# Kernel tuning notes

Hardware: AMD Instinct MI355X
Metric: run time of the kernel (lower is better)

Reference implementation:

```python
import jax, jax.numpy as jnp
import numpy as np
import math

HIDDEN = 1024
HEADS = 16
HEAD_DIM = HIDDEN // HEADS


def setup_inputs() -> dict:
    key = jax.random.key(0)
    ks = jax.random.split(key, 9)
    B, T, C = 4, 2048, HIDDEN
    s = 0.02
    x = jax.random.normal(ks[0], (B, T, C), dtype=jnp.float32)
    # torch nn.Linear weights are [out_features, in_features]
    Wq = jax.random.normal(ks[1], (C, C), dtype=jnp.float32) * s
    Wk = jax.random.normal(ks[2], (C, C), dtype=jnp.float32) * s
    Wv = jax.random.normal(ks[3], (C, C), dtype=jnp.float32) * s
    Wo = jax.random.normal(ks[4], (C, C), dtype=jnp.float32) * s
    bq = jax.random.normal(ks[5], (C,), dtype=jnp.float32) * s
    bk = jax.random.normal(ks[6], (C,), dtype=jnp.float32) * s
    bv = jax.random.normal(ks[7], (C,), dtype=jnp.float32) * s
    bo = jax.random.normal(ks[8], (C,), dtype=jnp.float32) * s
    return {"x": x, "Wq": Wq, "bq": bq, "Wk": Wk, "bk": bk,
            "Wv": Wv, "bv": bv, "Wo": Wo, "bo": bo}


def reference(x, Wq, bq, Wk, bk, Wv, bv, Wo, bo):
    B, T, C = x.shape
    H, D = HEADS, HEAD_DIM
    # projections: torch Linear => x @ W.T + b
    q = (x @ Wq.T + bq).reshape(B, T, H, D).transpose(0, 2, 1, 3)  # [B,H,T,D]
    k = (x @ Wk.T + bk).reshape(B, T, H, D).transpose(0, 2, 1, 3)
    v = (x @ Wv.T + bv).reshape(B, T, H, D).transpose(0, 2, 1, 3)
    scale = 1.0 / math.sqrt(D)
    scores = jnp.einsum('bhqd,bhkd->bhqk', q, k) * scale  # [B,H,T,T]
    attn = jax.nn.softmax(scores, axis=-1)
    y = jnp.einsum('bhqk,bhkd->bhqd', attn, v)  # [B,H,T,D]
    y = y.transpose(0, 2, 1, 3).reshape(B, T, C)
    return y @ Wo.T + bo
```

## Files before the change

kernel.cpp:

```cpp
#include <hip/hip_runtime.h>
#include <stdint.h>


using u16 = unsigned short;
using u32 = unsigned int;
typedef __attribute__((ext_vector_type(8))) __bf16 bf16x8;
typedef __attribute__((ext_vector_type(4))) float  floatx4;

#define QSCALE 0.18033688011112043f

__device__ __forceinline__ u16 f2b(float f) {
    union { float f; u32 i; } x; x.f = f;
    return (u16)((x.i + 0x7fffu + ((x.i >> 16) & 1u)) >> 16);
}
__device__ __forceinline__ u32 fbits(float f) { union { float f; u32 i; } x; x.f = f; return x.i; }
__device__ __forceinline__ u32 pkbf(float a, float b) {
    u32 ia = fbits(a) + 0x8000u, ib = fbits(b) + 0x8000u;
    return __builtin_amdgcn_perm(ib, ia, 0x07060302u);
}
__device__ __forceinline__ bf16x8 ld16B(const u16* p) {
    bf16x8 v; __builtin_memcpy(&v, p, 16); return v;
}
__device__ __forceinline__ void async16(const u16* g, u16* l) {
    __builtin_amdgcn_global_load_lds((const __attribute__((address_space(1))) unsigned int*)g,
                                     (__attribute__((address_space(3))) unsigned int*)l,
                                     16, 0, 0);
}

__global__ __launch_bounds__(256) void convert_kernel(
    const float* __restrict__ x,
    const float* __restrict__ Wq, const float* __restrict__ Wk,
    const float* __restrict__ Wv, const float* __restrict__ Wo,
    u16* __restrict__ xb, u16* __restrict__ wqb, u16* __restrict__ wkb,
    u16* __restrict__ wvb, u16* __restrict__ wob)
{
    size_t e = ((size_t)blockIdx.x * 256 + threadIdx.x) * 4;
    const float* src; u16* dst; size_t off;
    const size_t XN = (size_t)8 << 20;
    if (e < XN) { src = x; dst = xb; off = e; }
    else {
        size_t k = e - XN;
        int w = (int)(k >> 20);
        off = k & ((1u << 20) - 1);
        src = (w == 0) ? Wq : (w == 1) ? Wk : (w == 2) ? Wv : Wo;
        dst = (w == 0) ? wqb : (w == 1) ? wkb : (w == 2) ? wvb : wob;
    }
    float4 f = *(const float4*)(src + off);
    u32 dws[2] = { pkbf(f.x, f.y), pkbf(f.z, f.w) };
    __builtin_memcpy(dst + off, dws, 8);
}

template <int MODE, typename OutT>
__device__ __forceinline__ void gemm_bt_body(const u16* __restrict__ A,
                                             const u16* __restrict__ W,
                                             const float* __restrict__ bias,
                                             OutT* __restrict__ out,
                                             int m0, int n0, float scale)
{
    constexpr int K = 1024;
    __shared__ __align__(16) u16 sA[128 * 64];
    __shared__ __align__(16) u16 sB[128 * 64];

    const int tid  = threadIdx.x;
    const int wave = tid >> 6, lane = tid & 63;
    const int wr = wave >> 1, wc = wave & 1;
    const int quad = lane >> 4, l15 = lane & 15;

    floatx4 acc[4][4];
    #pragma unroll
    for (int i = 0; i < 4; ++i)
        #pragma unroll
        for (int j = 0; j < 4; ++j)
            acc[i][j] = (floatx4){0.f, 0.f, 0.f, 0.f};

    #pragma unroll 1
    for (int kb = 0; kb < 16; ++kb) {
        __syncthreads();
        const int k0 = kb * 64;
        #pragma unroll
        for (int j = 0; j < 4; ++j) {
            int r  = wave * 32 + j * 8 + (lane >> 3);
            int kg = (lane & 7) ^ (r & 7);
            async16(A + (size_t)(m0 + r) * K + k0 + kg * 8, &sA[(wave * 32 + j * 8) * 64]);
            async16(W + (size_t)(n0 + r) * K + k0 + kg * 8, &sB[(wave * 32 + j * 8) * 64]);
        }
        __syncthreads();

        #pragma unroll
        for (int kk = 0; kk < 2; ++kk) {
            bf16x8 af[4], bf[4];
            const int kg = kk * 4 + quad;
            #pragma unroll
            for (int t = 0; t < 4; ++t) {
                int ra = wr * 64 + t * 16 + l15;
                af[t] = ld16B(&sA[ra * 64 + ((kg ^ (ra & 7)) * 8)]);
                int rb = wc * 64 + t * 16 + l15;
                bf[t] = ld16B(&sB[rb * 64 + ((kg ^ (rb & 7)) * 8)]);
            }
            #pragma unroll
            for (int mt = 0; mt < 4; ++mt)
                #pragma unroll
                for (int nt = 0; nt < 4; ++nt)
                    acc[mt][nt] = __builtin_amdgcn_mfma_f32_16x16x32_bf16(af[mt], bf[nt], acc[mt][nt], 0, 0, 0);
        }
    }

    #pragma unroll
    for (int nt = 0; nt < 4; ++nt) {
        int col = n0 + wc * 64 + nt * 16 + l15;
        float bcol = (MODE == 1) ? 0.f : bias[col];
        #pragma unroll
        for (int mt = 0; mt < 4; ++mt) {
            #pragma unroll
            for (int r = 0; r < 4; ++r) {
                int row = m0 + wr * 64 + mt * 16 + quad * 4 + r;
                if (MODE == 1) {
                    float v = acc[mt][nt][r] + bias[row];
                    size_t idx = (((size_t)((col >> 11) * 16 + (row >> 6)) * 64 + (row & 63)) * 2048) + (col & 2047);
                    ((u16*)out)[idx] = f2b(v);
                } else if (MODE == 0) {
                    float v = (acc[mt][nt][r] + bcol) * scale;
                    ((u16*)out)[(size_t)row * 1024 + col] = f2b(v);
                } else {
                    ((float*)out)[(size_t)row * 1024 + col] = acc[mt][nt][r] + bcol;
                }
            }
        }
    }
}

__global__ __launch_bounds__(256) void qk_kernel(
    const u16* __restrict__ x,
    const u16* __restrict__ Wq, const u16* __restrict__ Wk,
    const float* __restrict__ bq, const float* __restrict__ bk,
    u16* __restrict__ q, u16* __restrict__ k)
{
    const int z = blockIdx.z;
    gemm_bt_body<0, u16>(x, z ? Wk : Wq, z ? bk : bq, z ? k : q,
                         blockIdx.y * 128, blockIdx.x * 128, z ? 1.0f : QSCALE);
}

__global__ __launch_bounds__(256) void v_kernel(
    const u16* __restrict__ x, const u16* __restrict__ Wv,
    const float* __restrict__ bv, u16* __restrict__ vt)
{
    gemm_bt_body<1, u16>(Wv, x, bv, vt, blockIdx.y * 128, blockIdx.x * 128, 1.0f);
}

__global__ __launch_bounds__(256) void proj_kernel(
    const u16* __restrict__ y, const u16* __restrict__ Wo, const float* __restrict__ bo,
    float* __restrict__ out)
{
    gemm_bt_body<2, float>(y, Wo, bo, out, blockIdx.y * 128, blockIdx.x * 128, 1.0f);
}

__global__ __launch_bounds__(256, 2) void attn_kernel(
    const u16* __restrict__ Q, const u16* __restrict__ K,
    const u16* __restrict__ Vt, u16* __restrict__ Y)
{
    const int bh = blockIdx.x, qt = blockIdx.y;
    const int tid = threadIdx.x;
    const int wave = tid >> 6, lane = tid & 63;
    const int quad = lane >> 4, l15 = lane & 15, l7 = l15 & 7;
    const int b = bh >> 4, h = bh & 15;

    __shared__ __align__(16) u16 sK[2][64 * 64];
    __shared__ __align__(16) u16 sV[2][64 * 64];
    __shared__ __align__(16) u16 sP[4][64 * 72];

    bf16x8 qf[4][2];
    #pragma unroll
    for (int nt = 0; nt < 4; ++nt) {
        const u16* qp = Q + (size_t)(b * 2048 + qt * 256 + wave * 64 + nt * 16 + l15) * 1024 + h * 64 + quad * 8;
        qf[nt][0] = ld16B(qp);
        qf[nt][1] = ld16B(qp + 32);
    }

    const int r8 = lane >> 3;
    const int g7 = (lane & 7) ^ r8;
    const u16* ksrc = K  + (size_t)(b * 2048 + wave * 16 + r8) * 1024 + h * 64 + g7 * 8;
    const u16* vsrc = Vt + ((size_t)(bh * 64 + wave * 16 + r8)) * 2048 + g7 * 8;

    floatx4 accO[4][4];
    #pragma unroll
    for (int mt = 0; mt < 4; ++mt)
        #pragma unroll
        for (int nt = 0; nt < 4; ++nt) accO[mt][nt] = (floatx4){0.f, 0.f, 0.f, 0.f};
    float rs[4] = {0.f, 0.f, 0.f, 0.f};

    {
        u16* dK = &sK[0][wave * 16 * 64];
        u16* dV = &sV[0][wave * 16 * 64];
        async16(ksrc,            dK);
        async16(ksrc + 8 * 1024, dK + 8 * 64);
        async16(vsrc,            dV);
        async16(vsrc + 8 * 2048, dV + 8 * 64);
    }
    __syncthreads();

    #pragma unroll 1
    for (int kt = 0; kt < 32; ++kt) {
        const int cur = kt & 1;
        if (kt < 31) {
            u16* dK = &sK[cur ^ 1][wave * 16 * 64];
            u16* dV = &sV[cur ^ 1][wave * 16 * 64];
            const u16* ks = ksrc + (size_t)(kt + 1) * 64 * 1024;
            const u16* vs = vsrc + (size_t)(kt + 1) * 64;
            async16(ks,            dK);
            async16(ks + 8 * 1024, dK + 8 * 64);
            async16(vs,            dV);
            async16(vs + 8 * 2048, dV + 8 * 64);
        }
        const u16* bK = sK[cur];
        const u16* bV = sV[cur];
        u16* sp = sP[wave];

        bf16x8 kf[4][2];
        #pragma unroll
        for (int mt = 0; mt < 4; ++mt)
            #pragma unroll
            for (int kk = 0; kk < 2; ++kk)
                kf[mt][kk] = ld16B(&bK[(mt * 16 + l15) * 64 + (((kk * 4 + quad) ^ l7) * 8)]);

        #pragma unroll
        for (int nt = 0; nt < 4; ++nt) {
            floatx4 st[4];
            #pragma unroll
            for (int mt = 0; mt < 4; ++mt) st[mt] = (floatx4){0.f, 0.f, 0.f, 0.f};
            #pragma unroll
            for (int kk = 0; kk < 2; ++kk)
                #pragma unroll
                for (int mt = 0; mt < 4; ++mt)
                    st[mt] = __builtin_amdgcn_mfma_f32_16x16x32_bf16(kf[mt][kk], qf[nt][kk], st[mt], 0, 0, 0);
            #pragma unroll
            for (int mt = 0; mt < 4; ++mt) {
                float p0 = __builtin_amdgcn_exp2f(st[mt][0]);
                float p1 = __builtin_amdgcn_exp2f(st[mt][1]);
                float p2 = __builtin_amdgcn_exp2f(st[mt][2]);
                float p3 = __builtin_amdgcn_exp2f(st[mt][3]);
                rs[nt] += (p0 + p1) + (p2 + p3);
                u32 dws[2] = { pkbf(p0, p1), pkbf(p2, p3) };
                __builtin_memcpy(&sp[(nt * 16 + l15) * 72 + mt * 16 + quad * 4], dws, 8);
            }
        }

        #pragma unroll
        for (int kk = 0; kk < 2; ++kk) {
            bf16x8 pf[4];
            #pragma unroll
            for (int nt = 0; nt < 4; ++nt)
                pf[nt] = ld16B(&sp[(nt * 16 + l15) * 72 + kk * 32 + quad * 8]);
            #pragma unroll
            for (int mt = 0; mt < 4; ++mt) {
                bf16x8 vf = ld16B(&bV[(mt * 16 + l15) * 64 + (((kk * 4 + quad) ^ l7) * 8)]);
                #pragma unroll
                for (int nt = 0; nt < 4; ++nt)
                    accO[mt][nt] = __builtin_amdgcn_mfma_f32_16x16x32_bf16(vf, pf[nt], accO[mt][nt], 0, 0, 0);
            }
        }
        __syncthreads();
    }

    float inv[4];
    #pragma unroll
    for (int nt = 0; nt < 4; ++nt) {
        float s = rs[nt];
        s += __shfl_xor(s, 16);
        s += __shfl_xor(s, 32);
        inv[nt] = 1.f / s;
    }
    u16* sp = sP[wave];
    #pragma unroll
    for (int nt = 0; nt < 4; ++nt)
        #pragma unroll
        for (int mt = 0; mt < 4; ++mt) {
            u32 dws[2] = { pkbf(accO[mt][nt][0] * inv[nt], accO[mt][nt][1] * inv[nt]),
                           pkbf(accO[mt][nt][2] * inv[nt], accO[mt][nt][3] * inv[nt]) };
            __builtin_memcpy(&sp[(nt * 16 + l15) * 72 + mt * 16 + quad * 4], dws, 8);
        }
    const int rl = lane >> 3, cl = lane & 7;
    #pragma unroll
    for (int pass = 0; pass < 8; ++pass) {
        int q = pass * 8 + rl;
        int t = qt * 256 + wave * 64 + q;
        bf16x8 vrow = ld16B(&sp[q * 72 + cl * 8]);
        __builtin_memcpy(Y + ((size_t)(b * 2048 + t)) * 1024 + h * 64 + cl * 8, &vrow, 16);
    }
}

extern "C" void kernel_launch(void* const* d_in, const int* in_sizes, int n_in,
                              void* d_out, int out_size, void* d_ws, size_t ws_size,
                              hipStream_t stream)
{
    const float* x  = (const float*)d_in[0];
    const float* Wq = (const float*)d_in[1];
    const float* bq = (const float*)d_in[2];
    const float* Wk = (const float*)d_in[3];
    const float* bk = (const float*)d_in[4];
    const float* Wv = (const float*)d_in[5];
    const float* bv = (const float*)d_in[6];
    const float* Wo = (const float*)d_in[7];
    const float* bo = (const float*)d_in[8];
    float* out = (float*)d_out;

    const size_t NTOK = (size_t)8192 * 1024;
    const size_t WN   = (size_t)1024 * 1024;
    u16* xb  = (u16*)d_ws;
    u16* wqb = xb + NTOK;
    u16* wkb = wqb + WN;
    u16* wvb = wkb + WN;
    u16* wob = wvb + WN;
    u16* q   = wob + WN;
    u16* k   = q + NTOK;
    u16* vt  = k + NTOK;
    u16* y   = vt + NTOK;

    convert_kernel<<<dim3(12288), 256, 0, stream>>>(x, Wq, Wk, Wv, Wo, xb, wqb, wkb, wvb, wob);
    qk_kernel<<<dim3(8, 64, 2), 256, 0, stream>>>(xb, wqb, wkb, bq, bk, q, k);
    v_kernel<<<dim3(64, 8), 256, 0, stream>>>(xb, wvb, bv, vt);
    attn_kernel<<<dim3(64, 8), 256, 0, stream>>>(q, k, vt, y);
    proj_kernel<<<dim3(8, 64), 256, 0, stream>>>(y, wob, bo, out);
}
```

Baseline: 276.3 us.

## Fuse QKV projections into one GEMM and compute softmax row sums via MFMA

Merges the separate Q/K and V projection kernels into a single launch over concatenated weights (relying on wq/wk/wv being contiguous in the workspace). V is now computed as x·Wv^T and stored transposed, with packed 8-byte stores in the epilogue. In attention, row sums are accumulated with an MFMA against a ones vector instead of scalar adds plus shuffles, and the P·V product is interleaved per query tile with V fragments preloaded. This trades fewer launches and less VALU work for extra MFMAs and higher register pressure, and the V stores now land with a different access pattern.

New measurement: 269.0 us. 1.03x faster.

```diff
diff --git a/kernel.cpp b/kernel.cpp
--- a/kernel.cpp
+++ b/kernel.cpp
@@ -50,23 +50,16 @@
     __builtin_memcpy(dst + off, dws, 8);
 }
 
-template <int MODE, typename OutT>
-__device__ __forceinline__ void gemm_bt_body(const u16* __restrict__ A,
-                                             const u16* __restrict__ W,
-                                             const float* __restrict__ bias,
-                                             OutT* __restrict__ out,
-                                             int m0, int n0, float scale)
+__device__ __forceinline__ void gemm_loop(const u16* __restrict__ A, const u16* __restrict__ W,
+                                          int m0, int n0, floatx4 (&acc)[4][4],
+                                          u16* __restrict__ sA, u16* __restrict__ sB)
 {
     constexpr int K = 1024;
-    __shared__ __align__(16) u16 sA[128 * 64];
-    __shared__ __align__(16) u16 sB[128 * 64];
-
     const int tid  = threadIdx.x;
     const int wave = tid >> 6, lane = tid & 63;
     const int wr = wave >> 1, wc = wave & 1;
     const int quad = lane >> 4, l15 = lane & 15;
 
-    floatx4 acc[4][4];
     #pragma unroll
     for (int i = 0; i < 4; ++i)
         #pragma unroll
@@ -104,54 +97,82 @@
                     acc[mt][nt] = __builtin_amdgcn_mfma_f32_16x16x32_bf16(af[mt], bf[nt], acc[mt][nt], 0, 0, 0);
         }
     }
+}
+
+__global__ __launch_bounds__(256) void qkv_kernel(
+    const u16* __restrict__ x, const u16* __restrict__ Wcat,
+    const float* __restrict__ bq, const float* __restrict__ bk, const float* __restrict__ bv,
+    u16* __restrict__ q, u16* __restrict__ k, u16* __restrict__ vt)
+{
+    __shared__ __align__(16) u16 sA[128 * 64];
+    __shared__ __align__(16) u16 sB[128 * 64];
+    const int m0 = blockIdx.y * 128, n0 = blockIdx.x * 128;
+    floatx4 acc[4][4];
+    gemm_loop(x, Wcat, m0, n0, acc, sA, sB);
+
+    const int tid = threadIdx.x;
+    const int wave = tid >> 6, lane = tid & 63;
+    const int wr = wave >> 1, wc = wave & 1;
+    const int quad = lane >> 4, l15 = lane & 15;
+
+    const int z = n0 >> 10;
+    const float* bb = (z == 0) ? bq : (z == 1) ? bk : bv;
+    const float scale = (z == 0) ? QSCALE : 1.0f;
+    u16* o = (z == 0) ? q : k;
 
     #pragma unroll
     for (int nt = 0; nt < 4; ++nt) {
-        int col = n0 + wc * 64 + nt * 16 + l15;
-        float bcol = (MODE == 1) ? 0.f : bias[col];
+        int col  = n0 + wc * 64 + nt * 16 + l15;
+        int c    = col & 1023;
+        float bv_ = bb[c];
         #pragma unroll
         for (int mt = 0; mt < 4; ++mt) {
-            #pragma unroll
-            for (int r = 0; r < 4; ++r) {
-                int row = m0 + wr * 64 + mt * 16 + quad * 4 + r;
-                if (MODE == 1) {
-                    float v = acc[mt][nt][r] + bias[row];
-                    size_t idx = (((size_t)((col >> 11) * 16 + (row >> 6)) * 64 + (row & 63)) * 2048) + (col & 2047);
-                    ((u16*)out)[idx] = f2b(v);
-                } else if (MODE == 0) {
-                    float v = (acc[mt][nt][r] + bcol) * scale;
-                    ((u16*)out)[(size_t)row * 1024 + col] = f2b(v);
-                } else {
-                    ((float*)out)[(size_t)row * 1024 + col] = acc[mt][nt][r] + bcol;
+            int row0 = m0 + wr * 64 + mt * 16 + quad * 4;
+            if (z == 2) {
+                float v0 = acc[mt][nt][0] + bv_, v1 = acc[mt][nt][1] + bv_;
+                float v2 = acc[mt][nt][2] + bv_, v3 = acc[mt][nt][3] + bv_;
+                u32 dws[2] = { pkbf(v0, v1), pkbf(v2, v3) };
+                int b = row0 >> 11, t0 = row0 & 2047;
+                size_t idx = ((size_t)((b * 16 + (c >> 6)) * 64 + (c & 63)) * 2048) + t0;
+                __builtin_memcpy(vt + idx, dws, 8);
+            } else {
+                #pragma unroll
+                for (int r = 0; r < 4; ++r) {
+                    float v = (acc[mt][nt][r] + bv_) * scale;
+                    o[(size_t)(row0 + r) * 1024 + c] = f2b(v);
                 }
             }
         }
     }
-}
-
-__global__ __launch_bounds__(256) void qk_kernel(
-    const u16* __restrict__ x,
-    const u16* __restrict__ Wq, const u16* __restrict__ Wk,
-    const float* __restrict__ bq, const float* __restrict__ bk,
-    u16* __restrict__ q, u16* __restrict__ k)
-{
-    const int z = blockIdx.z;
-    gemm_bt_body<0, u16>(x, z ? Wk : Wq, z ? bk : bq, z ? k : q,
-                         blockIdx.y * 128, blockIdx.x * 128, z ? 1.0f : QSCALE);
-}
-
-__global__ __launch_bounds__(256) void v_kernel(
-    const u16* __restrict__ x, const u16* __restrict__ Wv,
-    const float* __restrict__ bv, u16* __restrict__ vt)
-{
-    gemm_bt_body<1, u16>(Wv, x, bv, vt, blockIdx.y * 128, blockIdx.x * 128, 1.0f);
 }
 
 __global__ __launch_bounds__(256) void proj_kernel(
     const u16* __restrict__ y, const u16* __restrict__ Wo, const float* __restrict__ bo,
     float* __restrict__ out)
 {
-    gemm_bt_body<2, float>(y, Wo, bo, out, blockIdx.y * 128, blockIdx.x * 128, 1.0f);
+    __shared__ __align__(16) u16 sA[128 * 64];
+    __shared__ __align__(16) u16 sB[128 * 64];
+    const int m0 = blockIdx.y * 128, n0 = blockIdx.x * 128;
+    floatx4 acc[4][4];
+    gemm_loop(y, Wo, m0, n0, acc, sA, sB);
+
+    const int tid = threadIdx.x;
+    const int wave = tid >> 6, lane = tid & 63;
+    const int wr = wave >> 1, wc = wave & 1;
+    const int quad = lane >> 4, l15 = lane & 15;
+
+    #pragma unroll
+    for (int nt = 0; nt < 4; ++nt) {
+        int col = n0 + wc * 64 + nt * 16 + l15;
+        float bv_ = bo[col];
+        #pragma unroll
+        for (int mt = 0; mt < 4; ++mt) {
+            int row0 = m0 + wr * 64 + mt * 16 + quad * 4;
+            #pragma unroll
+            for (int r = 0; r < 4; ++r)
+                out[(size_t)(row0 + r) * 1024 + col] = acc[mt][nt][r] + bv_;
+        }
+    }
 }
 
 __global__ __launch_bounds__(256, 2) void attn_kernel(
@@ -168,6 +189,9 @@
     __shared__ __align__(16) u16 sV[2][64 * 64];
     __shared__ __align__(16) u16 sP[4][64 * 72];
 
+    const __bf16 one = (__bf16)1.0f;
+    const bf16x8 ones = { one, one, one, one, one, one, one, one };
+
     bf16x8 qf[4][2];
     #pragma unroll
     for (int nt = 0; nt < 4; ++nt) {
@@ -186,7 +210,9 @@
     for (int mt = 0; mt < 4; ++mt)
         #pragma unroll
         for (int nt = 0; nt < 4; ++nt) accO[mt][nt] = (floatx4){0.f, 0.f, 0.f, 0.f};
-    float rs[4] = {0.f, 0.f, 0.f, 0.f};
+    floatx4 accR[4];
+    #pragma unroll
+    for (int nt = 0; nt < 4; ++nt) accR[nt] = (floatx4){0.f, 0.f, 0.f, 0.f};
 
     {
         u16* dK = &sK[0][wave * 16 * 64];
@@ -197,6 +223,9 @@
         async16(vsrc + 8 * 2048, dV + 8 * 64);
     }
     __syncthreads();
+
+    u16* sp = sP[wave];
+    const int spRow = l15 * 72;
 
     #pragma unroll 1
     for (int kt = 0; kt < 32; ++kt) {
@@ -213,14 +242,15 @@
         }
         const u16* bK = sK[cur];
         const u16* bV = sV[cur];
-        u16* sp = sP[wave];
-
-        bf16x8 kf[4][2];
+
+        bf16x8 kf[4][2], vf[4][2];
         #pragma unroll
         for (int mt = 0; mt < 4; ++mt)
             #pragma unroll
-            for (int kk = 0; kk < 2; ++kk)
+            for (int kk = 0; kk < 2; ++kk) {
                 kf[mt][kk] = ld16B(&bK[(mt * 16 + l15) * 64 + (((kk * 4 + quad) ^ l7) * 8)]);
+                vf[mt][kk] = ld16B(&bV[(mt * 16 + l15) * 64 + (((kk * 4 + quad) ^ l7) * 8)]);
+            }
 
         #pragma unroll
         for (int nt = 0; nt < 4; ++nt) {
@@ -232,30 +262,25 @@
                 #pragma unroll
                 for (int mt = 0; mt < 4; ++mt)
                     st[mt] = __builtin_amdgcn_mfma_f32_16x16x32_bf16(kf[mt][kk], qf[nt][kk], st[mt], 0, 0, 0);
+
+            u16* spn = sp + nt * 16 * 72 + spRow;
             #pragma unroll
             for (int mt = 0; mt < 4; ++mt) {
                 float p0 = __builtin_amdgcn_exp2f(st[mt][0]);
                 float p1 = __builtin_amdgcn_exp2f(st[mt][1]);
                 float p2 = __builtin_amdgcn_exp2f(st[mt][2]);
                 float p3 = __builtin_amdgcn_exp2f(st[mt][3]);
-                rs[nt] += (p0 + p1) + (p2 + p3);
                 u32 dws[2] = { pkbf(p0, p1), pkbf(p2, p3) };
-                __builtin_memcpy(&sp[(nt * 16 + l15) * 72 + mt * 16 + quad * 4], dws, 8);
-            }
-        }
-
-        #pragma unroll
-        for (int kk = 0; kk < 2; ++kk) {
-            bf16x8 pf[4];
-            #pragma unroll
-            for (int nt = 0; nt < 4; ++nt)
-                pf[nt] = ld16B(&sp[(nt * 16 + l15) * 72 + kk * 32 + quad * 8]);
+                __builtin_memcpy(spn + mt * 16 + quad * 4, dws, 8);
+            }
+            bf16x8 pf0 = ld16B(spn + quad * 8);
+            bf16x8 pf1 = ld16B(spn + 32 + quad * 8);
+            accR[nt] = __builtin_amdgcn_mfma_f32_16x16x32_bf16(ones, pf0, accR[nt], 0, 0, 0);
+            accR[nt] = __builtin_amdgcn_mfma_f32_16x16x32_bf16(ones, pf1, accR[nt], 0, 0, 0);
             #pragma unroll
             for (int mt = 0; mt < 4; ++mt) {
-                bf16x8 vf = ld16B(&bV[(mt * 16 + l15) * 64 + (((kk * 4 + quad) ^ l7) * 8)]);
-                #pragma unroll
-                for (int nt = 0; nt < 4; ++nt)
-                    accO[mt][nt] = __builtin_amdgcn_mfma_f32_16x16x32_bf16(vf, pf[nt], accO[mt][nt], 0, 0, 0);
+                accO[mt][nt] = __builtin_amdgcn_mfma_f32_16x16x32_bf16(vf[mt][0], pf0, accO[mt][nt], 0, 0, 0);
+                accO[mt][nt] = __builtin_amdgcn_mfma_f32_16x16x32_bf16(vf[mt][1], pf1, accO[mt][nt], 0, 0, 0);
             }
         }
         __syncthreads();
@@ -263,13 +288,7 @@
 
     float inv[4];
     #pragma unroll
-    for (int nt = 0; nt < 4; ++nt) {
-        float s = rs[nt];
-        s += __shfl_xor(s, 16);
-        s += __shfl_xor(s, 32);
-        inv[nt] = 1.f / s;
-    }
-    u16* sp = sP[wave];
+    for (int nt = 0; nt < 4; ++nt) inv[nt] = 1.f / accR[nt][0];
     #pragma unroll
     for (int nt = 0; nt < 4; ++nt)
         #pragma unroll
@@ -281,9 +300,9 @@
     const int rl = lane >> 3, cl = lane & 7;
     #pragma unroll
     for (int pass = 0; pass < 8; ++pass) {
-        int q = pass * 8 + rl;
-        int t = qt * 256 + wave * 64 + q;
-        bf16x8 vrow = ld16B(&sp[q * 72 + cl * 8]);
+        int qq = pass * 8 + rl;
+        int t = qt * 256 + wave * 64 + qq;
+        bf16x8 vrow = ld16B(&sp[qq * 72 + cl * 8]);
         __builtin_memcpy(Y + ((size_t)(b * 2048 + t)) * 1024 + h * 64 + cl * 8, &vrow, 16);
     }
 }
@@ -316,8 +335,7 @@
     u16* y   = vt + NTOK;
 
     convert_kernel<<<dim3(12288), 256, 0, stream>>>(x, Wq, Wk, Wv, Wo, xb, wqb, wkb, wvb, wob);
-    qk_kernel<<<dim3(8, 64, 2), 256, 0, stream>>>(xb, wqb, wkb, bq, bk, q, k);
-    v_kernel<<<dim3(64, 8), 256, 0, stream>>>(xb, wvb, bv, vt);
+    qkv_kernel<<<dim3(24, 64), 256, 0, stream>>>(xb, wqb, bq, bk, bv, q, k, vt);
     attn_kernel<<<dim3(64, 8), 256, 0, stream>>>(q, k, vt, y);
     proj_kernel<<<dim3(8, 64), 256, 0, stream>>>(y, wob, bo, out);
 }
```
